# Kernel optimization log

Hardware: AMD Instinct MI355X
Metric: run time of the kernel (lower is better)

The kernel has to match this reference:

```python
import jax, jax.numpy as jnp
import numpy as np

B, L, DM = 4, 2048, 1024  # batch, seq len (== l_max, global kernel), d_model; head_dim = 1


def setup_inputs() -> dict:
    key = jax.random.key(0)
    ks = jax.random.split(key, 13)
    n = lambda k, shape, s=1.0: jax.random.normal(k, shape, dtype=jnp.float32) * s
    W_SCALE = 0.02   # keeps activations well-conditioned through the chained convs
    K_SCALE = 0.02
    return {
        "u": n(ks[0], (B, L, DM)),
        "Wq": n(ks[1], (DM, DM), W_SCALE), "bq": n(ks[2], (DM,), W_SCALE),
        "Wk": n(ks[3], (DM, DM), W_SCALE), "bk": n(ks[4], (DM,), W_SCALE),
        "Wv": n(ks[5], (DM, DM), W_SCALE), "bv": n(ks[6], (DM,), W_SCALE),
        "k_kernel": n(ks[7], (DM, L), K_SCALE),
        "k_D": n(ks[8], (DM,)),
        "ssm_kernel": n(ks[9], (DM, L), K_SCALE),
        "D": n(ks[10], (DM,)),
        "Wo": n(ks[11], (DM, DM), W_SCALE), "bo": n(ks[12], (DM,), W_SCALE),
    }


def reference(u, Wq, bq, Wk, bk, Wv, bv, k_kernel, k_D, ssm_kernel, D, Wo, bo):
    # u: (B, L, H) with H = d_model (head_dim = 1)
    Lseq = u.shape[1]
    fft_size = 2 * Lseq  # zero-pad to 2L for linear (causal) convolution

    # q/k/v projections -> (B, H, L)
    q = jnp.einsum('blh,dh->bdl', u, Wq) + bq[None, :, None]
    k = jnp.einsum('blh,dh->bdl', u, Wk) + bk[None, :, None]
    v = jnp.einsum('blh,dh->bdl', u, Wv) + bv[None, :, None]

    # shift conv on k: k <- k_kernel * k (causal FFT conv) + k_D * k
    k_kernel_f = jnp.fft.rfft(k_kernel, n=fft_size)           # (H, F)
    k_f = jnp.fft.rfft(k, n=fft_size)                          # (B, H, F)
    shift_k = jnp.fft.irfft(k_kernel_f[None] * k_f, n=fft_size)[..., :Lseq]
    k = shift_k + k_D[None, :, None] * k

    # head_dim == 1: kv outer product collapses to elementwise gate
    kv = k * v                                                 # (B, H, L)

    # ssm conv on kv (torch's 1/fft_size + norm='forward' irfft == standard irfft)
    kv_f = jnp.fft.rfft(kv, n=fft_size)                        # (B, H, F)
    ssm_kernel_f = jnp.fft.rfft(ssm_kernel, n=fft_size)        # (H, F)
    y = jnp.fft.irfft(kv_f * ssm_kernel_f[None], n=fft_size)[..., :Lseq]
    y = y + kv * D[None, :, None]                              # D skip

    # q gating, then output projection
    y = y * q                                                  # (B, H, L)
    y = jnp.swapaxes(y, 1, 2)                                  # (B, L, H)
    return jnp.einsum('blh,oh->blo', y, Wo) + bo
```

## Files before the change

kernel.cpp:

```cpp
#include <hip/hip_runtime.h>
#include <hip/hip_bf16.h>
#include <stdint.h>

#define DM   1024
#define LSEQ 2048
#define NB   4

typedef __attribute__((ext_vector_type(8))) short  short8;
typedef __attribute__((ext_vector_type(4))) float  floatx4;

__device__ __forceinline__ ushort f2b(float x) {
    union { float f; uint32_t u; } v; v.f = x;
    uint32_t b = v.u + 0x7FFF + ((v.u >> 16) & 1);
    return (ushort)(b >> 16);
}
__device__ __forceinline__ float b2f(ushort x) {
    union { uint32_t u; float f; } v; v.u = ((uint32_t)x) << 16;
    return v.f;
}

__global__ __launch_bounds__(256) void cvt_all_kernel(const float* __restrict__ u,
                                                      const float* __restrict__ Wq,
                                                      const float* __restrict__ Wk,
                                                      const float* __restrict__ Wv,
                                                      const float* __restrict__ Wo,
                                                      ushort* __restrict__ U16,
                                                      ushort* __restrict__ Wcat) {
    const int nu  = NB * LSEQ * DM / 8;
    const int per = DM * DM / 8;
    int i = blockIdx.x * 256 + threadIdx.x;
    const float* src; ushort* dst; int j;
    if (i < nu) { src = u; dst = U16; j = i; }
    else {
        int k = i - nu;
        int r = k / per;
        src = (r == 0) ? Wq : (r == 1) ? Wk : (r == 2) ? Wv : Wo;
        dst = Wcat + (size_t)r * (DM * DM);
        j = k - r * per;
    }
    const float4* p = (const float4*)src + (size_t)j * 2;
    float4 a = p[0], b = p[1];
    union { ushort us[8]; uint4 v; } o;
    o.us[0] = f2b(a.x); o.us[1] = f2b(a.y); o.us[2] = f2b(a.z); o.us[3] = f2b(a.w);
    o.us[4] = f2b(b.x); o.us[5] = f2b(b.y); o.us[6] = f2b(b.z); o.us[7] = f2b(b.w);
    *(uint4*)(dst + (size_t)j * 8) = o.v;
}

template <int MODE, int BN>
__global__ __launch_bounds__(512, 2) void gemm_v2(const ushort* __restrict__ Aw,
                                                  const ushort* __restrict__ Bw,
                                                  const float* __restrict__ b0,
                                                  const float* __restrict__ b1,
                                                  const float* __restrict__ b2,
                                                  void* __restrict__ C0v,
                                                  void* __restrict__ C1v,
                                                  void* __restrict__ C2v,
                                                  int N, int nbx) {
    constexpr int K = 1024, BK = 64, NT = K / BK;
    constexpr int BM     = 128;
    constexpr int NJH    = BN / 128;
    constexpr int ASLOT  = BM * 128;
    constexpr int BSLOT  = BN * 128;
    constexpr int BOFF   = 2 * ASLOT;
    __shared__ char lds[BOFF + 2 * BSLOT];

    const int tid   = threadIdx.x;
    const int wave  = tid >> 6;
    const int lane  = tid & 63;
    const int qlane = lane & 15;
    const int qk    = lane >> 4;
    const int z7    = qlane & 7;
    const int wm    = wave >> 2;
    const int wn    = wave & 3;

    int flat = blockIdx.y * nbx + blockIdx.x;
    int nwg  = nbx * gridDim.y;
    int swz  = (flat & 7) * (nwg >> 3) + (flat >> 3);
    const int tn = (swz % nbx) * BN;
    const int tm = (swz / nbx) * BM;

    const int srcChunkOff = ((lane & 7) ^ (lane >> 3)) * 8;
    const int srcRow      = lane >> 3;

#define STAGE_A(TT)                                                                           \
    {                                                                                         \
        const int trow = tm + wave * 16 + srcRow;                                             \
        char* dst = lds + ((TT) & 1) * ASLOT + wave * 2048;                                   \
        const int k0_ = (TT) * BK;                                                            \
        _Pragma("unroll")                                                                     \
        for (int j = 0; j < 2; ++j) {                                                         \
            const ushort* src = Aw + (size_t)(trow + j * 8) * K + k0_ + srcChunkOff;          \
            __builtin_amdgcn_global_load_lds(                                                 \
                (const __attribute__((address_space(1))) void*)src,                           \
                (__attribute__((address_space(3))) void*)(dst + j * 1024), 16, 0, 0);         \
        }                                                                                     \
    }
#define STAGE_B(TT, H)                                                                        \
    {                                                                                         \
        const int rbase = (H) * (BN / 2) + wave * (8 * NJH);                                  \
        const int trow  = tn + rbase + srcRow;                                                \
        char* dst = lds + BOFF + ((TT) & 1) * BSLOT + rbase * 128;                            \
        const int k0_ = (TT) * BK;                                                            \
        _Pragma("unroll")                                                                     \
        for (int j = 0; j < NJH; ++j) {                                                       \
            const ushort* src = Bw + (size_t)(trow + j * 8) * K + k0_ + srcChunkOff;          \
            __builtin_amdgcn_global_load_lds(                                                 \
                (const __attribute__((address_space(1))) void*)src,                           \
                (__attribute__((address_space(3))) void*)(dst + j * 1024), 16, 0, 0);         \
        }                                                                                     \
    }

    short8 afA[4][2], afB[4][2], bf0[NJH][2], bf1[NJH][2];
    floatx4 acc[2][4][NJH] = {};

#define LDA(TT, AF)                                                                           \
    {                                                                                         \
        const char* Ab = lds + ((TT) & 1) * ASLOT;                                            \
        _Pragma("unroll")                                                                     \
        for (int i = 0; i < 4; ++i) {                                                         \
            int lr = wm * 64 + i * 16 + qlane;                                                \
            _Pragma("unroll")                                                                 \
            for (int ks = 0; ks < 2; ++ks)                                                    \
                AF[i][ks] = *(const short8*)(Ab + lr * 128 + (((ks * 4 + qk) ^ z7) << 4));    \
        }                                                                                     \
    }
#define LDB(TT, NH, BF)                                                                       \
    {                                                                                         \
        const char* Bb = lds + BOFF + ((TT) & 1) * BSLOT;                                     \
        _Pragma("unroll")                                                                     \
        for (int j = 0; j < NJH; ++j) {                                                       \
            int lr = wn * (BN / 4) + (NH) * (NJH * 16) + j * 16 + qlane;                      \
            _Pragma("unroll")                                                                 \
            for (int ks = 0; ks < 2; ++ks)                                                    \
                BF[j][ks] = *(const short8*)(Bb + lr * 128 + (((ks * 4 + qk) ^ z7) << 4));    \
        }                                                                                     \
    }
#define MFMAQ(NH, AF, BF)                                                                     \
    __builtin_amdgcn_s_setprio(1);                                                           \
    _Pragma("unroll")                                                                         \
    for (int ks = 0; ks < 2; ++ks)                                                            \
        _Pragma("unroll")                                                                     \
        for (int i = 0; i < 4; ++i)                                                           \
            _Pragma("unroll")                                                                 \
            for (int j = 0; j < NJH; ++j)                                                     \
                acc[NH][i][j] = __builtin_amdgcn_mfma_f32_16x16x32_bf16(                      \
                    AF[i][ks], BF[j][ks], acc[NH][i][j], 0, 0, 0);                            \
    __builtin_amdgcn_s_setprio(0);
#define BARX  __builtin_amdgcn_s_barrier(); __builtin_amdgcn_sched_barrier(0)
#define VM_STEADY                                                                             \
    do { if constexpr (BN == 384) asm volatile("s_waitcnt vmcnt(8)" ::: "memory");            \
         else                     asm volatile("s_waitcnt vmcnt(6)" ::: "memory"); } while (0)

    STAGE_A(0); STAGE_B(0, 0); STAGE_B(0, 1);
    STAGE_A(1); STAGE_B(1, 0); STAGE_B(1, 1);
    VM_STEADY;
    BARX;
    LDA(0, afA); LDB(0, 0, bf0);
    asm volatile("s_waitcnt lgkmcnt(0)" ::: "memory");
    __builtin_amdgcn_sched_barrier(0);
    BARX;

#define TILE(T, AFc, AFn)                                                                     \
    {                                                                                         \
        LDB(T, 1, bf1);                                                                       \
        MFMAQ(0, AFc, bf0);                                                                   \
        BARX;                                                                                 \
        if ((T) + 2 < NT) { STAGE_A((T) + 2); STAGE_B((T) + 2, 0); STAGE_B((T) + 2, 1); }     \
        MFMAQ(1, AFc, bf1);                                                                   \
        if ((T) + 2 < NT)      { VM_STEADY; }                                                 \
        else if ((T) + 1 < NT) { asm volatile("s_waitcnt vmcnt(0)" ::: "memory"); }           \
        BARX;                                                                                 \
        if ((T) + 1 < NT) { LDA((T) + 1, AFn); LDB((T) + 1, 0, bf0); }                        \
    }

    for (int t = 0; t < NT; t += 2) {
        TILE(t,     afA, afB);
        TILE(t + 1, afB, afA);
    }
#undef TILE
#undef STAGE_A
#undef STAGE_B
#undef LDA
#undef LDB
#undef MFMAQ
#undef BARX
#undef VM_STEADY

#pragma unroll
    for (int nh = 0; nh < 2; ++nh)
#pragma unroll
    for (int i = 0; i < 4; ++i)
#pragma unroll
    for (int j = 0; j < NJH; ++j) {
        int n  = tn + wn * (BN / 4) + nh * (NJH * 16) + j * 16 + qlane;
        int m0 = tm + wm * 64 + i * 16 + qk * 4;
        if (MODE == 0) {
            int proj = n >> 10, dd = n & (DM - 1);
            const float* bb = (proj == 0) ? b0 : (proj == 1) ? b1 : b2;
            ushort* Cb      = (ushort*)((proj == 0) ? C0v : (proj == 1) ? C1v : C2v);
            float bv = bb[dd];
            int b = m0 >> 11, l = m0 & (LSEQ - 1);
            ushort4 val;
            val.x = f2b(acc[nh][i][j][0] + bv);
            val.y = f2b(acc[nh][i][j][1] + bv);
            val.z = f2b(acc[nh][i][j][2] + bv);
            val.w = f2b(acc[nh][i][j][3] + bv);
            *(ushort4*)(Cb + ((size_t)b * DM + dd) * LSEQ + l) = val;
        } else {
            float* C0 = (float*)C0v;
            float bv = b0[n];
#pragma unroll
            for (int r = 0; r < 4; ++r)
                C0[(size_t)(m0 + r) * N + n] = acc[nh][i][j][r] + bv;
        }
    }
}

#define KSTR 2096
#define XSTR 2248

__global__ __launch_bounds__(256, 4) void conv_fused_kernel(const ushort* __restrict__ x,
                                                            const float* __restrict__ ker1,
                                                            const float* __restrict__ scale1,
                                                            const ushort* __restrict__ gate1,
                                                            const float* __restrict__ ker2,
                                                            const float* __restrict__ scale2,
                                                            const ushort* __restrict__ gate2,
                                                            ushort* __restrict__ out) {
    __shared__ ushort krev1[KSTR];
    __shared__ ushort krev2[KSTR];
    __shared__ ushort xs[4 * XSTR];
    const int d    = blockIdx.x;
    const int tid  = threadIdx.x;
    const int wave = tid >> 6;
    const int lane = tid & 63;

    {
        const ushort* src = x + ((size_t)wave * DM + d) * LSEQ + lane * 8;
        char* dst = (char*)xs + wave * (XSTR * 2) + 256;
#pragma unroll
        for (int c = 0; c < 4; ++c)
            __builtin_amdgcn_global_load_lds((const __attribute__((address_space(1))) void*)(src + c * 512),
                                             (__attribute__((address_space(3))) void*)(dst + c * 1024),
                                             16, 0, 0);
    }
    {
        int e0 = tid * 8;
        const float* k1p = ker1 + (size_t)d * LSEQ + e0;
        const float* k2p = ker2 + (size_t)d * LSEQ + e0;
        float4 a1 = *(const float4*)(k1p),     b1 = *(const float4*)(k1p + 4);
        float4 a2 = *(const float4*)(k2p),     b2 = *(const float4*)(k2p + 4);
        ushort4 o;
        o.x = f2b(a1.w); o.y = f2b(a1.z); o.z = f2b(a1.y); o.w = f2b(a1.x);
        *(ushort4*)(krev1 + (2060 - e0)) = o;
        o.x = f2b(b1.w); o.y = f2b(b1.z); o.z = f2b(b1.y); o.w = f2b(b1.x);
        *(ushort4*)(krev1 + (2056 - e0)) = o;
        o.x = f2b(a2.w); o.y = f2b(a2.z); o.z = f2b(a2.y); o.w = f2b(a2.x);
        *(ushort4*)(krev2 + (2060 - e0)) = o;
        o.x = f2b(b2.w); o.y = f2b(b2.z); o.z = f2b(b2.y); o.w = f2b(b2.x);
        *(ushort4*)(krev2 + (2056 - e0)) = o;
        uint4 z = {0, 0, 0, 0};
        if (tid < 2) {
            *(uint4*)((char*)krev1 + tid * 16) = z;
            *(uint4*)((char*)krev2 + tid * 16) = z;
        }
        if (tid >= 2 && tid < 6) {
            *(uint4*)((char*)krev1 + 4128 + (tid - 2) * 16) = z;
            *(uint4*)((char*)krev2 + 4128 + (tid - 2) * 16) = z;
        }
        if (tid >= 64 && tid < 128) {
            int b = (tid - 64) >> 4, c = (tid - 64) & 15;
            *(uint4*)((char*)xs + b * (XSTR * 2) + c * 16) = z;
        }
        if (tid >= 128 && tid < 144) {
            int b = (tid - 128) >> 2, c = (tid - 128) & 3;
            *(uint4*)((char*)xs + b * (XSTR * 2) + 4352 + c * 16) = z;
        }
    }
    __syncthreads();

    const int qn = lane & 15;
    const int qk = lane >> 4;

    int g[4] = {wave, 7 - wave, 8 + wave, 15 - wave};
    const int smax_all = 128 * (15 - wave) + 128;

    const int lbase = (qn & 3) * XSTR + 128 + 16 * (qn >> 2) + 8 * qk;

#define CSTEP(KR, ACC, SS, FP)                                                               \
    {                                                                                        \
        int b_el = 2063 - qn + 8 * qk - (SS);                                                \
        int A0 = b_el & ~1;                                                                  \
        uint sh = (uint)(b_el & 1) * 16u;                                                    \
        uint e0 = *(const uint*)((KR) + A0);                                                 \
        uint e1 = *(const uint*)((KR) + A0 + 2);                                             \
        uint e2 = *(const uint*)((KR) + A0 + 4);                                             \
        uint e3 = *(const uint*)((KR) + A0 + 6);                                             \
        uint e4 = *(const uint*)((KR) + A0 + 8);                                             \
        union { uint u[4]; short8 v; } Af;                                                   \
        Af.u[0] = __builtin_amdgcn_alignbit(e1, e0, sh);                                     \
        Af.u[1] = __builtin_amdgcn_alignbit(e2, e1, sh);                                     \
        Af.u[2] = __builtin_amdgcn_alignbit(e3, e2, sh);                                     \
        Af.u[3] = __builtin_amdgcn_alignbit(e4, e3, sh);                                     \
        _Pragma("unroll")                                                                    \
        for (int gi = 0; gi < 4; ++gi) {                                                     \
            if ((SS) <= 128 * g[gi] + 128) {                                                 \
                short8 fN = *(const short8*)(xs + lbase + 128 * g[gi] - (SS));               \
                ACC[gi][0] = __builtin_amdgcn_mfma_f32_16x16x32_bf16(Af.v, fN, ACC[gi][0], 0, 0, 0); \
                ACC[gi][1] = __builtin_amdgcn_mfma_f32_16x16x32_bf16(Af.v, FP[gi], ACC[gi][1], 0, 0, 0); \
                FP[gi] = fN;                                                                 \
            }                                                                                \
        }                                                                                    \
    }

    {
        floatx4 acc[4][2] = {};
        short8 fE[4], fO[4];
#pragma unroll
        for (int gi = 0; gi < 4; ++gi) {
            fE[gi] = *(const short8*)(xs + lbase + 128 * g[gi] + 64);
            fO[gi] = *(const short8*)(xs + lbase + 128 * g[gi] + 32);
        }
        for (int s = 0; s <= smax_all; s += 64) {
            CSTEP(krev1, acc, s, fE);
            if (s + 32 <= smax_all) CSTEP(krev1, acc, s + 32, fO);
        }

        __syncthreads();
        const float sc = scale1[d];
#pragma unroll
        for (int gi = 0; gi < 4; ++gi) {
#pragma unroll
            for (int m = 0; m < 2; ++m) {
                int p  = 8 * g[gi] + 4 * m + (qn >> 2);
                int b  = qn & 3;
                int l0 = 16 * p + 4 * qk;
                size_t off = ((size_t)b * DM + d) * LSEQ + l0;
                ushort4 xv = *(const ushort4*)(xs + b * XSTR + 128 + l0);
                ushort4 gv = *(const ushort4*)(gate1 + off);
                ushort4 ov;
                ov.x = f2b((acc[gi][m][0] + sc * b2f(xv.x)) * b2f(gv.x));
                ov.y = f2b((acc[gi][m][1] + sc * b2f(xv.y)) * b2f(gv.y));
                ov.z = f2b((acc[gi][m][2] + sc * b2f(xv.z)) * b2f(gv.z));
                ov.w = f2b((acc[gi][m][3] + sc * b2f(xv.w)) * b2f(gv.w));
                *(ushort4*)(xs + b * XSTR + 128 + l0) = ov;
            }
        }
        __syncthreads();
    }

    {
        floatx4 acc[4][2] = {};
        short8 fE[4], fO[4];
#pragma unroll
        for (int gi = 0; gi < 4; ++gi) {
            fE[gi] = *(const short8*)(xs + lbase + 128 * g[gi] + 64);
            fO[gi] = *(const short8*)(xs + lbase + 128 * g[gi] + 32);
        }
        for (int s = 0; s <= smax_all; s += 64) {
            CSTEP(krev2, acc, s, fE);
            if (s + 32 <= smax_all) CSTEP(krev2, acc, s + 32, fO);
        }

        const float sc = scale2[d];
#pragma unroll
        for (int gi = 0; gi < 4; ++gi) {
#pragma unroll
            for (int m = 0; m < 2; ++m) {
                int p  = 8 * g[gi] + 4 * m + (qn >> 2);
                int b  = qn & 3;
                int l0 = 16 * p + 4 * qk;
                size_t off = ((size_t)b * DM + d) * LSEQ + l0;
                ushort4 xv = *(const ushort4*)(xs + b * XSTR + 128 + l0);
                ushort4 gv = *(const ushort4*)(gate2 + off);
                ushort4 ov;
                ov.x = f2b((acc[gi][m][0] + sc * b2f(xv.x)) * b2f(gv.x));
                ov.y = f2b((acc[gi][m][1] + sc * b2f(xv.y)) * b2f(gv.y));
                ov.z = f2b((acc[gi][m][2] + sc * b2f(xv.z)) * b2f(gv.z));
                ov.w = f2b((acc[gi][m][3] + sc * b2f(xv.w)) * b2f(gv.w));
                *(ushort4*)(out + off) = ov;
            }
        }
    }
#undef CSTEP
}

__global__ __launch_bounds__(256) void transpose_bf16(const ushort* __restrict__ in,
                                                      ushort* __restrict__ out) {
    __shared__ ushort t[32][36];
    const int l0 = blockIdx.x * 32;
    const int d0 = blockIdx.y * 32;
    const int b  = blockIdx.z;
    const int q  = threadIdx.x & 7;
    const int r  = threadIdx.x >> 3;
    *(ushort4*)(&t[r][q * 4]) = *(const ushort4*)(in + ((size_t)b * DM + d0 + r) * LSEQ + l0 + q * 4);
    __syncthreads();
    ushort4 o;
    o.x = t[q * 4 + 0][r]; o.y = t[q * 4 + 1][r]; o.z = t[q * 4 + 2][r]; o.w = t[q * 4 + 3][r];
    *(ushort4*)(out + ((size_t)b * LSEQ + l0 + r) * DM + d0 + q * 4) = o;
}

extern "C" void kernel_launch(void* const* d_in, const int* in_sizes, int n_in,
                              void* d_out, int out_size, void* d_ws, size_t ws_size,
                              hipStream_t stream) {
    const float* u        = (const float*)d_in[0];
    const float* Wq       = (const float*)d_in[1];
    const float* bq       = (const float*)d_in[2];
    const float* Wk       = (const float*)d_in[3];
    const float* bk       = (const float*)d_in[4];
    const float* Wv       = (const float*)d_in[5];
    const float* bv       = (const float*)d_in[6];
    const float* k_kernel = (const float*)d_in[7];
    const float* k_D      = (const float*)d_in[8];
    const float* ssm_ker  = (const float*)d_in[9];
    const float* Dv       = (const float*)d_in[10];
    const float* Wo       = (const float*)d_in[11];
    const float* bo       = (const float*)d_in[12];
    float* outp = (float*)d_out;

    char* ws = (char*)d_ws;
    ushort* Q    = (ushort*)(ws);
    ushort* KV   = (ushort*)(ws + (16ull << 20));
    ushort* V    = (ushort*)(ws + (32ull << 20));
    ushort* U16  = (ushort*)(ws + (48ull << 20));
    ushort* YT   = (ushort*)(ws + (64ull << 20));
    ushort* Wcat = (ushort*)(ws + (80ull << 20));

    const int nu = NB * LSEQ * DM / 8, nw = 4 * DM * DM / 8;
    cvt_all_kernel<<<(nu + nw) / 256, 256, 0, stream>>>(u, Wq, Wk, Wv, Wo, U16, Wcat);

    dim3 g1(3 * DM / 384, NB * LSEQ / 128);
    gemm_v2<0, 384><<<g1, 512, 0, stream>>>(U16, Wcat, bq, bk, bv, Q, KV, V,
                                            3 * DM, 3 * DM / 384);

    conv_fused_kernel<<<DM, 256, 0, stream>>>(KV, k_kernel, k_D, V, ssm_ker, Dv, Q, KV);

    dim3 g2(LSEQ / 32, DM / 32, NB);
    transpose_bf16<<<g2, 256, 0, stream>>>(KV, YT);

    dim3 g3(DM / 256, NB * LSEQ / 128);
    gemm_v2<1, 256><<<g3, 512, 0, stream>>>(YT, Wcat + 3 * DM * DM, bo, bo, bo,
                                            outp, outp, outp, DM, DM / 256);
}
```

Measured before the change: 156.4 us.

## Add double-buffered BK=32 GEMM kernel for QKV projection with direct-to-LDS loads

Replaces the templated QKV projection GEMM with a new kernel that uses 128x256 tiles, BK=32, and double-buffered LDS staging through global_load_lds. MFMA work is split into halves so the next tile's global loads and LDS fragment reads overlap with compute, and MFMA issue priority is raised. An XOR swizzle is applied to avoid LDS bank conflicts. The change also moves from 384- to 256-column tiles, which gives more workgroups but smaller per-block reuse and more barriers per K.

```diff
diff --git a/kernel.cpp b/kernel.cpp
--- a/kernel.cpp
+++ b/kernel.cpp
@@ -44,6 +44,141 @@
     o.us[0] = f2b(a.x); o.us[1] = f2b(a.y); o.us[2] = f2b(a.z); o.us[3] = f2b(a.w);
     o.us[4] = f2b(b.x); o.us[5] = f2b(b.y); o.us[6] = f2b(b.z); o.us[7] = f2b(b.w);
     *(uint4*)(dst + (size_t)j * 8) = o.v;
+}
+
+__global__ __launch_bounds__(512, 2) void gemm_v4(const ushort* __restrict__ Aw,
+                                                  const ushort* __restrict__ Bw,
+                                                  const float* __restrict__ b0,
+                                                  const float* __restrict__ b1,
+                                                  const float* __restrict__ b2,
+                                                  ushort* __restrict__ C0,
+                                                  ushort* __restrict__ C1,
+                                                  ushort* __restrict__ C2,
+                                                  int N, int nbx) {
+    constexpr int K = 1024, BK = 32, NT = K / BK;
+    constexpr int ASLOT = 128 * 64;
+    constexpr int BSLOT = 256 * 64;
+    constexpr int BOFF  = 2 * ASLOT;
+    __shared__ char lds[BOFF + 2 * BSLOT];
+
+    const int tid   = threadIdx.x;
+    const int wave  = tid >> 6;
+    const int lane  = tid & 63;
+    const int qlane = lane & 15;
+    const int qk    = lane >> 4;
+    const int z3    = qlane & 3;
+    const int wm    = wave >> 2;
+    const int wn    = wave & 3;
+
+    int flat = blockIdx.y * nbx + blockIdx.x;
+    int nwg  = nbx * gridDim.y;
+    int swz  = (flat & 7) * (nwg >> 3) + (flat >> 3);
+    const int tn = (swz % nbx) * 256;
+    const int tm = (swz / nbx) * 128;
+
+    const int srcChunkOff = (((lane & 3) ^ ((lane >> 2) & 3)) * 8);
+    const int srcRow      = lane >> 2;
+
+#define STAGE4(TT)                                                                           \
+    {                                                                                        \
+        const int k0_ = (TT) * BK;                                                           \
+        {                                                                                    \
+            const int trow = tm + wave * 16 + srcRow;                                        \
+            const ushort* src = Aw + (size_t)trow * K + k0_ + srcChunkOff;                   \
+            __builtin_amdgcn_global_load_lds(                                                \
+                (const __attribute__((address_space(1))) void*)src,                          \
+                (__attribute__((address_space(3))) void*)(lds + ((TT) & 1) * ASLOT +         \
+                                                          wave * 1024), 16, 0, 0);           \
+        }                                                                                    \
+        _Pragma("unroll")                                                                    \
+        for (int jj = 0; jj < 2; ++jj) {                                                     \
+            const int trow = tn + wave * 32 + jj * 16 + srcRow;                              \
+            const ushort* src = Bw + (size_t)trow * K + k0_ + srcChunkOff;                   \
+            __builtin_amdgcn_global_load_lds(                                                \
+                (const __attribute__((address_space(1))) void*)src,                          \
+                (__attribute__((address_space(3))) void*)(lds + BOFF + ((TT) & 1) * BSLOT +  \
+                                                          wave * 2048 + jj * 1024), 16, 0, 0); \
+        }                                                                                    \
+    }
+
+    short8 afA[4], afB[4], bfA[4], bfB[4];
+    floatx4 acc[4][4] = {};
+
+#define LD4A(TT, AF)                                                                         \
+    {                                                                                        \
+        const char* Ab = lds + ((TT) & 1) * ASLOT;                                           \
+        _Pragma("unroll")                                                                    \
+        for (int i = 0; i < 4; ++i)                                                          \
+            AF[i] = *(const short8*)(Ab + (wm * 64 + i * 16 + qlane) * 64 +                  \
+                                     ((qk ^ z3) << 4));                                      \
+    }
+#define LD4B(TT, BF)                                                                         \
+    {                                                                                        \
+        const char* Bb = lds + BOFF + ((TT) & 1) * BSLOT;                                    \
+        _Pragma("unroll")                                                                    \
+        for (int j = 0; j < 4; ++j)                                                          \
+            BF[j] = *(const short8*)(Bb + (wn * 64 + j * 16 + qlane) * 64 +                  \
+                                     ((qk ^ z3) << 4));                                      \
+    }
+#define MFMAQ4(H, AF, BF)                                                                    \
+    __builtin_amdgcn_s_setprio(1);                                                          \
+    _Pragma("unroll")                                                                        \
+    for (int i = 0; i < 4; ++i)                                                              \
+        _Pragma("unroll")                                                                    \
+        for (int j = 2 * (H); j < 2 * (H) + 2; ++j)                                          \
+            acc[i][j] = __builtin_amdgcn_mfma_f32_16x16x32_bf16(AF[i], BF[j], acc[i][j], 0, 0, 0); \
+    __builtin_amdgcn_s_setprio(0);
+#define BARX  __builtin_amdgcn_s_barrier(); __builtin_amdgcn_sched_barrier(0)
+
+    STAGE4(0); STAGE4(1);
+    asm volatile("s_waitcnt vmcnt(3)" ::: "memory");
+    BARX;
+    LD4A(0, afA); LD4B(0, bfA);
+    asm volatile("s_waitcnt lgkmcnt(0)" ::: "memory");
+    __builtin_amdgcn_sched_barrier(0);
+    BARX;
+
+#define TILE4(T, AFc, BFc, AFn, BFn)                                                         \
+    {                                                                                        \
+        MFMAQ4(0, AFc, BFc);                                                                 \
+        BARX;                                                                                \
+        if ((T) + 2 < NT) STAGE4((T) + 2);                                                   \
+        MFMAQ4(1, AFc, BFc);                                                                 \
+        if ((T) + 2 < NT)      { asm volatile("s_waitcnt vmcnt(3)" ::: "memory"); }          \
+        else if ((T) + 1 < NT) { asm volatile("s_waitcnt vmcnt(0)" ::: "memory"); }          \
+        BARX;                                                                                \
+        if ((T) + 1 < NT) { LD4A((T) + 1, AFn); LD4B((T) + 1, BFn); }                        \
+    }
+
+    for (int t = 0; t < NT; t += 2) {
+        TILE4(t,     afA, bfA, afB, bfB);
+        TILE4(t + 1, afB, bfB, afA, bfA);
+    }
+#undef TILE4
+#undef STAGE4
+#undef LD4A
+#undef LD4B
+#undef MFMAQ4
+#undef BARX
+
+#pragma unroll
+    for (int i = 0; i < 4; ++i)
+#pragma unroll
+    for (int j = 0; j < 4; ++j) {
+        int n  = tn + wn * 64 + j * 16 + qlane;
+        int m0 = tm + wm * 64 + i * 16 + qk * 4;
+        int proj = n >> 10, dd = n & (DM - 1);
+        const float* bb = (proj == 0) ? b0 : (proj == 1) ? b1 : b2;
+        ushort* Cb      = (proj == 0) ? C0 : (proj == 1) ? C1 : C2;
+        float bv = bb[dd];
+        int b = m0 >> 11, l = m0 & (LSEQ - 1);
+        ushort4 val;
+        val.x = f2b(acc[i][j][0] + bv);
+        val.y = f2b(acc[i][j][1] + bv);
+        val.z = f2b(acc[i][j][2] + bv);
+        val.w = f2b(acc[i][j][3] + bv);
+        *(ushort4*)(Cb + ((size_t)b * DM + dd) * LSEQ + l) = val;
+    }
 }
 
 template <int MODE, int BN>
@@ -429,9 +564,9 @@
     const int nu = NB * LSEQ * DM / 8, nw = 4 * DM * DM / 8;
     cvt_all_kernel<<<(nu + nw) / 256, 256, 0, stream>>>(u, Wq, Wk, Wv, Wo, U16, Wcat);
 
-    dim3 g1(3 * DM / 384, NB * LSEQ / 128);
-    gemm_v2<0, 384><<<g1, 512, 0, stream>>>(U16, Wcat, bq, bk, bv, Q, KV, V,
-                                            3 * DM, 3 * DM / 384);
+    dim3 g1(3 * DM / 256, NB * LSEQ / 128);
+    gemm_v4<<<g1, 512, 0, stream>>>(U16, Wcat, bq, bk, bv, Q, KV, V,
+                                    3 * DM, 3 * DM / 256);
 
     conv_fused_kernel<<<DM, 256, 0, stream>>>(KV, k_kernel, k_D, V, ssm_ker, Dv, Q, KV);
 
```

Result: no change. 158.0 us (+1.0%).
